# Kernel optimization log

Hardware: AMD Instinct MI355X
Metric: run time of the kernel (lower is better)

## Reference

```python
import jax, jax.numpy as jnp
import numpy as np

B, T, D = 2, 1024, 1024
H = 8            # num_heads
DK = 128         # head_k_dim
DV = 128         # head_v_dim
M = 128          # num_slots (== head_k_dim by default)
K = 32           # topk
EPS = 1e-5
SCALE = 1.0


def _rmsnorm(x, w, eps=EPS):
    return x * jax.lax.rsqrt(jnp.mean(x * x, axis=-1, keepdims=True) + eps) * w


def setup_inputs() -> dict:
    key = jax.random.key(0)
    ks = jax.random.split(key, 12)
    def lin(k, fan_in, fan_out):
        return jax.random.normal(k, (fan_in, fan_out), jnp.float32) / np.sqrt(fan_in).astype(np.float32)
    hidden_states = jax.random.normal(ks[0], (B, T, D), jnp.float32)
    Wq = lin(ks[1], D, H * DK)
    Wk = lin(ks[2], D, H * DK)
    Wv = lin(ks[3], D, H * DV)
    Wr = lin(ks[4], D, H * M)
    Wa = lin(ks[5], D, H)
    # Mamba2-style decay params
    A_log = jnp.log(jax.random.uniform(ks[6], (H,), jnp.float32, 1e-3, 16.0))
    dt = jnp.exp(jax.random.uniform(ks[7], (H,), jnp.float32) * (np.log(0.1) - np.log(0.001)) + np.log(0.001))
    dt = jnp.clip(dt, 1e-4, None)
    dt_bias = dt + jnp.log(-jnp.expm1(-dt))
    q_norm_w = jnp.ones((DK,), jnp.float32) + 0.01 * jax.random.normal(ks[8], (DK,), jnp.float32)
    k_norm_w = jnp.ones((DK,), jnp.float32) + 0.01 * jax.random.normal(ks[9], (DK,), jnp.float32)
    g_norm_w = jnp.ones((D,), jnp.float32) + 0.01 * jax.random.normal(ks[10], (D,), jnp.float32)
    Wo = lin(ks[11], H * DV, D)
    return dict(hidden_states=hidden_states, Wq=Wq, Wk=Wk, Wv=Wv, Wr=Wr, Wa=Wa,
                A_log=A_log, dt_bias=dt_bias, q_norm_w=q_norm_w, k_norm_w=k_norm_w,
                g_norm_w=g_norm_w, Wo=Wo)


def reference(hidden_states, Wq, Wk, Wv, Wr, Wa, A_log, dt_bias, q_norm_w, k_norm_w, g_norm_w, Wo):
    b, t, d = hidden_states.shape
    # projections
    q = (hidden_states @ Wq).reshape(b, t, H, DK)
    k = (hidden_states @ Wk).reshape(b, t, H, DK)
    v = jax.nn.silu((hidden_states @ Wv).reshape(b, t, H, DV))
    router = (hidden_states @ Wr).reshape(b, t, H, M)
    # Mamba2 decay (log-space, per head)
    f_head = -jnp.exp(A_log) * jax.nn.softplus(hidden_states @ Wa + dt_bias)  # [b,t,H]
    # swish feature map + per-head RMSNorm
    q = _rmsnorm(jax.nn.silu(q), q_norm_w)
    k = _rmsnorm(jax.nn.silu(k), k_norm_w)
    # sigmoid router scores, top-k slot routing (eval: no gumbel noise)
    scores = jax.nn.sigmoid(router)                    # [b,t,H,M]
    top_w, top_i = jax.lax.top_k(scores, K)            # [b,t,H,K]
    top_w = top_w / (jnp.sum(top_w, axis=-1, keepdims=True) + 1e-9)
    n = b * t * H
    rows = jnp.arange(n)[:, None]
    s_multihot = jnp.zeros((n, M), scores.dtype).at[rows, top_i.reshape(n, K)].set(
        top_w.reshape(n, K)).reshape(b, t, H, M)
    f = f_head[..., None] * s_multihot                 # [b,t,H,M], log decay per slot
    s = 1.0 - jnp.exp(f)                               # write gate per slot
    # decayed linear-attention recurrence over slots (M == DK):
    #   S_t[i,j] = exp(f_t[i]) * S_{t-1}[i,j] + s_t[i]*k_t[i]*v_t[j]
    #   o_t[j]   = scale * sum_i q_t[i] * S_t[i,j]
    def step(S, xs):
        q_t, k_t, v_t, f_t, s_t = xs                   # [b,H,*]
        S = jnp.exp(f_t)[..., None] * S + (s_t * k_t)[..., None] * v_t[..., None, :]
        o_t = jnp.einsum('bhk,bhkv->bhv', q_t, S) * SCALE
        return S, o_t
    xs = tuple(jnp.swapaxes(a, 0, 1) for a in (q, k, v, f, s))  # time-major
    S0 = jnp.zeros((b, H, DK, DV), q.dtype)
    _, o = jax.lax.scan(step, S0, xs)                  # o: [t,b,H,DV]
    o = jnp.swapaxes(o, 0, 1).reshape(b, t, H * DV)
    o = _rmsnorm(o, g_norm_w)                          # g_norm over hidden_size
    return o @ Wo
```

## Files before the change

kernel.cpp:

```cpp
#include <hip/hip_runtime.h>
#include <stdint.h>
#include <stddef.h>

#define H_ 8
#define T_ 1024

typedef __attribute__((ext_vector_type(8))) short s16x8;
typedef __attribute__((ext_vector_type(4))) float f32x4;
typedef __attribute__((ext_vector_type(16))) float f32x16;

static __device__ __forceinline__ unsigned short f2bf(float f){
  unsigned u = __float_as_uint(f);
  u += 0x7fffu + ((u >> 16) & 1u);
  return (unsigned short)(u >> 16);
}
static __device__ __forceinline__ float bf2f(unsigned short b){
  return __uint_as_float(((unsigned)b) << 16);
}
static __device__ __forceinline__ unsigned int pack_hl(float x){
  unsigned short h = f2bf(x);
  unsigned short l = f2bf(x - bf2f(h));
  return ((unsigned int)h << 16) | l;
}
static __device__ __forceinline__ void gl_lds16(const unsigned short* g, unsigned short* l){
  __builtin_amdgcn_global_load_lds((const __attribute__((address_space(1))) unsigned int*)g,
                                   (__attribute__((address_space(3))) unsigned int*)l,
                                   16, 0, 0);
}

__global__ void prep_k(const float* __restrict__ X, const float* __restrict__ Wa,
                       const float* __restrict__ A_log, const float* __restrict__ dtb,
                       unsigned short* __restrict__ hi, unsigned short* __restrict__ lo,
                       float* __restrict__ fh){
  __shared__ float xs[1024];
  int n = blockIdx.x, tid = threadIdx.x;
  size_t base = (size_t)n*1024 + tid*4;
  float4 x = *(const float4*)&X[base];
  *(float4*)&xs[tid*4] = x;
  float v[4] = {x.x,x.y,x.z,x.w};
  ushort4 h4, l4;
  unsigned short hh[4], ll[4];
#pragma unroll
  for(int j=0;j<4;j++){ hh[j]=f2bf(v[j]); ll[j]=f2bf(v[j]-bf2f(hh[j])); }
  h4.x=hh[0];h4.y=hh[1];h4.z=hh[2];h4.w=hh[3];
  l4.x=ll[0];l4.y=ll[1];l4.z=ll[2];l4.w=ll[3];
  *(ushort4*)&hi[base] = h4;
  *(ushort4*)&lo[base] = l4;
  __syncthreads();
  int h = tid>>5, l = tid&31;
  float s = 0.f;
  for(int k=l;k<1024;k+=32) s += xs[k]*Wa[(size_t)k*8 + h];
  s += __shfl_xor(s,1); s += __shfl_xor(s,2); s += __shfl_xor(s,4);
  s += __shfl_xor(s,8); s += __shfl_xor(s,16);
  if(l==0){
    float z = s + dtb[h];
    float sp = (z > 20.f) ? z : log1pf(expf(z));
    fh[(size_t)n*8 + h] = -expf(A_log[h]) * sp;
  }
}

__global__ void wtrans(const float* __restrict__ Wq, const float* __restrict__ Wk,
                       const float* __restrict__ Wv, const float* __restrict__ Wr,
                       const float* __restrict__ Wo,
                       unsigned short* __restrict__ WcatT3, unsigned short* __restrict__ WrThi,
                       unsigned short* __restrict__ WrTlo, unsigned short* __restrict__ WoT){
  __shared__ float tile[32][33];
  int z = blockIdx.z;
  const float* src = (z==0)?Wq:(z==1)?Wk:(z==2)?Wv:(z==3)?Wr:Wo;
  int c0 = blockIdx.x*32;
  int k0 = blockIdx.y*32;
  int tx = threadIdx.x, ty = threadIdx.y;
#pragma unroll
  for(int r=0;r<32;r+=8)
    tile[ty+r][tx] = src[(size_t)(k0+ty+r)*1024 + c0 + tx];
  __syncthreads();
#pragma unroll
  for(int r=0;r<32;r+=8){
    int c = c0 + ty + r;
    int k = k0 + tx;
    float v = tile[tx][ty+r];
    if(z < 3){
      WcatT3[((size_t)(z*1024 + c))*1024 + k] = f2bf(v);
    } else if(z == 3){
      unsigned short hv = f2bf(v);
      WrThi[(size_t)c*1024 + k] = hv;
      WrTlo[(size_t)c*1024 + k] = f2bf(v - bf2f(hv));
    } else {
      WoT[(size_t)c*1024 + k] = f2bf(v);
    }
  }
}

__launch_bounds__(256)
__global__ void gemm_fused(const unsigned short* __restrict__ Xhi, const unsigned short* __restrict__ Xlo,
                           const unsigned short* __restrict__ WcatT3, const unsigned short* __restrict__ WrThi,
                           const unsigned short* __restrict__ WrTlo,
                           float* __restrict__ C1, float* __restrict__ Rp){
  __shared__ unsigned short As[128*64];
  __shared__ unsigned short Bs[128*64];
  int bid = blockIdx.x;
  int blk = (bid&7)*96 + (bid>>3);
  const unsigned short *Ap, *Bp;
  float* Cout;
  int bx, by, N;
  if(blk < 384){
    bx = blk%24; by = blk/24; N = 3072;
    Ap = Xhi; Bp = WcatT3; Cout = C1;
  } else {
    int rb = blk-384;
    int seg = rb>>7, t2 = rb&127;
    bx = t2&7; by = t2>>3; N = 1024;
    Ap = (seg==2) ? Xlo : Xhi;
    Bp = (seg==1) ? WrTlo : WrThi;
    Cout = Rp + (size_t)seg*2048*1024;
  }
  int tid = threadIdx.x;
  int mBase = by*128, nBase = bx*128;
  int w = tid>>6, lane = tid&63, wr = w>>1, wc = w&1;
  int kg = lane>>4, l15 = lane&15;
  f32x4 acc[4][4];
#pragma unroll
  for(int i=0;i<4;i++)
#pragma unroll
    for(int j=0;j<4;j++) acc[i][j] = (f32x4){0.f,0.f,0.f,0.f};
  size_t aoff[4], boff[4];
#pragma unroll
  for(int p=0;p<4;p++){
    int c = p*256 + tid;
    int row = c>>3, sc = c&7, c8 = sc ^ (row&7);
    aoff[p] = (size_t)(mBase+row)*1024 + c8*8;
    boff[p] = (size_t)(nBase+row)*1024 + c8*8;
  }
  for(int kb=0; kb<1024; kb+=64){
#pragma unroll
    for(int p=0;p<4;p++){
      gl_lds16(Ap + aoff[p] + kb, &As[(p*256+tid)*8]);
      gl_lds16(Bp + boff[p] + kb, &Bs[(p*256+tid)*8]);
    }
    __syncthreads();
#pragma unroll
    for(int kk=0;kk<2;kk++){
      s16x8 afr[4], bfr[4];
#pragma unroll
      for(int f=0;f<4;f++){
        int rA = wr*64 + f*16 + l15;
        int rB = wc*64 + f*16 + l15;
        int cA = (kk*4 + kg) ^ (rA&7);
        int cB = (kk*4 + kg) ^ (rB&7);
        afr[f] = *(const s16x8*)&As[rA*64 + cA*8];
        bfr[f] = *(const s16x8*)&Bs[rB*64 + cB*8];
      }
#pragma unroll
      for(int fm=0;fm<4;fm++)
#pragma unroll
        for(int fn=0;fn<4;fn++)
          acc[fm][fn] = __builtin_amdgcn_mfma_f32_16x16x32_bf16(afr[fm], bfr[fn], acc[fm][fn], 0,0,0);
    }
    __syncthreads();
  }
#pragma unroll
  for(int fm=0;fm<4;fm++)
#pragma unroll
    for(int fn=0;fn<4;fn++){
      int col = nBase + wc*64 + fn*16 + l15;
      int row = mBase + wr*64 + fm*16 + kg*4;
#pragma unroll
      for(int r=0;r<4;r++) Cout[(size_t)(row+r)*N + col] = acc[fm][fn][r];
    }
}

__launch_bounds__(256)
__global__ void gemm_out(const unsigned short* __restrict__ A,
                         const unsigned short* __restrict__ BT,
                         float* __restrict__ C){
  __shared__ unsigned short As[128*64];
  __shared__ unsigned short Bs[64*64];
  const int K = 1024, N = 1024;
  int tid = threadIdx.x;
  int mBase = blockIdx.y*128, nBase = blockIdx.x*64;
  int w = tid>>6, lane = tid&63;
  int mh = w>>1, nh = w&1;
  int kg = lane>>4, l15 = lane&15;
  f32x4 acc[4][2];
#pragma unroll
  for(int i=0;i<4;i++)
#pragma unroll
    for(int j=0;j<2;j++) acc[i][j] = (f32x4){0.f,0.f,0.f,0.f};
  size_t aoff[4], boff[2];
#pragma unroll
  for(int p=0;p<4;p++){
    int c = p*256 + tid;
    int row = c>>3, sc = c&7, c8 = sc ^ (row&7);
    aoff[p] = (size_t)(mBase+row)*K + c8*8;
  }
#pragma unroll
  for(int p=0;p<2;p++){
    int c = p*256 + tid;
    int row = c>>3, sc = c&7, c8 = sc ^ (row&7);
    boff[p] = (size_t)(nBase+row)*K + c8*8;
  }
  for(int kb=0; kb<K; kb+=64){
#pragma unroll
    for(int p=0;p<4;p++) gl_lds16(A + aoff[p] + kb, &As[(p*256+tid)*8]);
#pragma unroll
    for(int p=0;p<2;p++) gl_lds16(BT + boff[p] + kb, &Bs[(p*256+tid)*8]);
    __syncthreads();
#pragma unroll
    for(int kk=0;kk<2;kk++){
      s16x8 afr[4], bfr[2];
#pragma unroll
      for(int f=0;f<4;f++){
        int r = mh*64 + f*16 + l15;
        afr[f] = *(const s16x8*)&As[r*64 + ((kk*4+kg) ^ (r&7))*8];
      }
#pragma unroll
      for(int f=0;f<2;f++){
        int r = nh*32 + f*16 + l15;
        bfr[f] = *(const s16x8*)&Bs[r*64 + ((kk*4+kg) ^ (r&7))*8];
      }
#pragma unroll
      for(int fm=0;fm<4;fm++)
#pragma unroll
        for(int fn=0;fn<2;fn++)
          acc[fm][fn] = __builtin_amdgcn_mfma_f32_16x16x32_bf16(afr[fm], bfr[fn], acc[fm][fn], 0,0,0);
    }
    __syncthreads();
  }
#pragma unroll
  for(int fm=0;fm<4;fm++)
#pragma unroll
    for(int fn=0;fn<2;fn++){
      int col = nBase + nh*32 + fn*16 + l15;
      int row = mBase + mh*64 + fm*16 + kg*4;
#pragma unroll
      for(int r=0;r<4;r++) C[(size_t)(row+r)*N + col] = acc[fm][fn][r];
    }
}

__launch_bounds__(256)
__global__ void postproc(const float* __restrict__ C1, const float* __restrict__ Rp,
                         const float* __restrict__ fh, const float* __restrict__ qw,
                         const float* __restrict__ kw,
                         float* __restrict__ Qd, float* __restrict__ Wt,
                         float* __restrict__ Fd, float* __restrict__ Vd){
  __shared__ unsigned long long keys[8][128];
  int n = blockIdx.x;
  int t = threadIdx.x;
  int b = n>>10, tt = n&1023;
  int h = t>>5;
  int i0 = (t&31)*4;
  size_t cb = (size_t)n*3072;
  size_t rbase = (size_t)n*1024 + h*128 + i0;
  float4 q4 = *(const float4*)&C1[cb + h*128 + i0];
  float4 k4 = *(const float4*)&C1[cb + 1024 + h*128 + i0];
  float4 v4 = *(const float4*)&C1[cb + 2048 + h*128 + i0];
  float4 r0 = *(const float4*)&Rp[rbase];
  float4 r1 = *(const float4*)&Rp[2048ull*1024 + rbase];
  float4 r2 = *(const float4*)&Rp[2ull*2048*1024 + rbase];
  float qv[4] = {q4.x,q4.y,q4.z,q4.w};
  float kv[4] = {k4.x,k4.y,k4.z,k4.w};
  float vv4[4] = {v4.x,v4.y,v4.z,v4.w};
  float rl[4] = {r0.x+r1.x+r2.x, r0.y+r1.y+r2.y, r0.z+r1.z+r2.z, r0.w+r1.w+r2.w};
  float qs[4], ks[4], vv[4], si[4];
  unsigned long long ki[4];
#pragma unroll
  for(int j=0;j<4;j++){
    qs[j] = qv[j]/(1.f+expf(-qv[j]));
    ks[j] = kv[j]/(1.f+expf(-kv[j]));
    vv[j] = vv4[j]/(1.f+expf(-vv4[j]));
    si[j] = 1.f/(1.f+expf(-rl[j]));
    ki[j] = (((unsigned long long)__float_as_uint(si[j])) << 7) | (unsigned)(127 - (i0+j));
    keys[h][i0+j] = ki[j];
  }
  __syncthreads();
  int cnt[4] = {0,0,0,0};
#pragma unroll 4
  for(int j=0;j<128;j+=2){
    ulonglong2 k2 = *(const ulonglong2*)&keys[h][j];
#pragma unroll
    for(int m=0;m<4;m++){
      cnt[m] += (k2.x > ki[m]);
      cnt[m] += (k2.y > ki[m]);
    }
  }
  bool sel[4];
#pragma unroll
  for(int m=0;m<4;m++) sel[m] = cnt[m] < 32;
  float x;
  x = qs[0]*qs[0]+qs[1]*qs[1]+qs[2]*qs[2]+qs[3]*qs[3];
  x+=__shfl_xor(x,1);x+=__shfl_xor(x,2);x+=__shfl_xor(x,4);x+=__shfl_xor(x,8);x+=__shfl_xor(x,16);
  float qrms = rsqrtf(x/128.f + 1e-5f);
  x = ks[0]*ks[0]+ks[1]*ks[1]+ks[2]*ks[2]+ks[3]*ks[3];
  x+=__shfl_xor(x,1);x+=__shfl_xor(x,2);x+=__shfl_xor(x,4);x+=__shfl_xor(x,8);x+=__shfl_xor(x,16);
  float krms = rsqrtf(x/128.f + 1e-5f);
  x = (sel[0]?si[0]:0.f)+(sel[1]?si[1]:0.f)+(sel[2]?si[2]:0.f)+(sel[3]?si[3]:0.f);
  x+=__shfl_xor(x,1);x+=__shfl_xor(x,2);x+=__shfl_xor(x,4);x+=__shfl_xor(x,8);x+=__shfl_xor(x,16);
  float winv = 1.f/(x + 1e-9f);
  float fhv = fh[(size_t)n*8 + h];
  size_t base = ((size_t)((b*H_ + h)*T_) + tt)*128 + i0;
  float4 qo, wo, fo, vo;
  float qd[4], wd[4], fd[4];
#pragma unroll
  for(int j=0;j<4;j++){
    float wgt = sel[j] ? si[j]*winv : 0.f;
    float f = fhv * wgt;
    qd[j] = qs[j]*qrms*qw[i0+j];
    wd[j] = (1.f - expf(f)) * (ks[j]*krms*kw[i0+j]);
    fd[j] = f;
  }
  qo.x=qd[0];qo.y=qd[1];qo.z=qd[2];qo.w=qd[3];
  wo.x=wd[0];wo.y=wd[1];wo.z=wd[2];wo.w=wd[3];
  fo.x=fd[0];fo.y=fd[1];fo.z=fd[2];fo.w=fd[3];
  vo.x=vv[0];vo.y=vv[1];vo.z=vv[2];vo.w=vv[3];
  *(float4*)&Qd[base] = qo;
  *(float4*)&Wt[base] = wo;
  *(float4*)&Fd[base] = fo;
  *(float4*)&Vd[base] = vo;
}

__launch_bounds__(256)
__global__ void chunk_sum(float* __restrict__ Fd, const float* __restrict__ Wt,
                          const float* __restrict__ Vd, float* __restrict__ dS,
                          float* __restrict__ E){
  __shared__ float Fc[32][132];
  __shared__ float Kh[32][132];
  int blk = blockIdx.x, bh = blk>>5, c = blk&31;
  int tid = threadIdx.x;
  int w = tid>>6, lane = tid&63;
  size_t fbase = ((size_t)bh*T_ + (size_t)c*32)*128;
#pragma unroll
  for(int v=0; v<4; v++){
    int e = v*1024 + tid*4;
    int t2 = e>>7, i0 = e&127;
    float4 f4 = *(const float4*)&Fd[fbase + e];
    *(float4*)&Fc[t2][i0] = f4;
  }
  __syncthreads();
  if(tid < 128){
    float a = 0.f;
    for(int t2=0;t2<32;t2++){ a += Fc[t2][tid]; Fc[t2][tid] = a; }
  }
  __syncthreads();
#pragma unroll
  for(int v=0; v<4; v++){
    int e = v*1024 + tid*4;
    int t2 = e>>7, i0 = e&127;
    float4 fc4 = *(const float4*)&Fc[t2][i0];
    *(float4*)&Fd[fbase + e] = fc4;
    float4 ft  = *(const float4*)&Fc[31][i0];
    float4 w4  = *(const float4*)&Wt[fbase + e];
    float4 kh;
    kh.x = w4.x * expf(ft.x - fc4.x);
    kh.y = w4.y * expf(ft.y - fc4.y);
    kh.z = w4.z * expf(ft.z - fc4.z);
    kh.w = w4.w * expf(ft.w - fc4.w);
    *(float4*)&Kh[t2][i0] = kh;
  }
  if(tid < 128) E[((size_t)bh*32 + c)*128 + tid] = expf(Fc[31][tid]);
  __syncthreads();
  int ig = lane>>3, jg = lane&7;
  const float* Vp = Vd + fbase;
  f32x4 acc[4][4];
#pragma unroll
  for(int a=0;a<4;a++)
#pragma unroll
    for(int q=0;q<4;q++) acc[a][q] = (f32x4){0.f,0.f,0.f,0.f};
#pragma unroll 4
  for(int t2=0;t2<32;t2++){
    float4 kq = *(const float4*)&Kh[t2][w*32 + ig*4];
    float4 v0 = *(const float4*)&Vp[t2*128 + jg*4];
    float4 v1 = *(const float4*)&Vp[t2*128 + jg*4 + 32];
    float4 v2 = *(const float4*)&Vp[t2*128 + jg*4 + 64];
    float4 v3 = *(const float4*)&Vp[t2*128 + jg*4 + 96];
    float kk[4] = {kq.x,kq.y,kq.z,kq.w};
#pragma unroll
    for(int a=0;a<4;a++){
      acc[a][0] += kk[a]*(f32x4){v0.x,v0.y,v0.z,v0.w};
      acc[a][1] += kk[a]*(f32x4){v1.x,v1.y,v1.z,v1.w};
      acc[a][2] += kk[a]*(f32x4){v2.x,v2.y,v2.z,v2.w};
      acc[a][3] += kk[a]*(f32x4){v3.x,v3.y,v3.z,v3.w};
    }
  }
  size_t dbase = (size_t)blk*16384;
#pragma unroll
  for(int q=0;q<4;q++)
#pragma unroll
    for(int jj=0;jj<4;jj++){
      float4 o4 = make_float4(acc[0][q][jj],acc[1][q][jj],acc[2][q][jj],acc[3][q][jj]);
      *(float4*)&dS[dbase + (size_t)(jg*4 + 32*q + jj)*128 + w*32 + ig*4] = o4;
    }
}

__global__ void scan_k(float* __restrict__ dS, const float* __restrict__ E){
  int g = blockIdx.x*256 + threadIdx.x;
  int bh = g>>12;
  int e4 = (g&4095)*4;
  int i0 = e4 & 127;
  float4 S = make_float4(0.f,0.f,0.f,0.f);
  for(int c=0;c<32;c++){
    size_t off = ((size_t)(bh*32 + c))*16384 + e4;
    float4 d   = *(const float4*)&dS[off];
    float4 Ec  = *(const float4*)&E[((size_t)(bh*32 + c))*128 + i0];
    *(float4*)&dS[off] = S;
    S.x = Ec.x*S.x + d.x;
    S.y = Ec.y*S.y + d.y;
    S.z = Ec.z*S.z + d.z;
    S.w = Ec.w*S.w + d.w;
  }
}

__launch_bounds__(256)
__global__ void chunk_out(const float* __restrict__ Qd, const float* __restrict__ Wt,
                          const float* __restrict__ Fd, const float* __restrict__ Vd,
                          const float* __restrict__ ST, float* __restrict__ O){
  __shared__ unsigned int qtP[32][132];
  __shared__ unsigned int ktP[32][132];
  __shared__ unsigned int Vt[128][36];
  __shared__ float Amat[32][40];
  int blk = blockIdx.x, bh = blk>>5, c = blk&31;
  int b = bh>>3, h = bh&7;
  int tid = threadIdx.x, w = tid>>6, lane = tid&63;
  int m = lane&31, hi = lane>>5;
  size_t fbase = ((size_t)bh*T_ + (size_t)c*32)*128;
#pragma unroll
  for(int p=0;p<4;p++){
    int e = p*1024 + tid*4;
    int t2 = e>>7, i0 = e&127;
    float4 f4 = *(const float4*)&Fd[fbase + e];
    float4 q4 = *(const float4*)&Qd[fbase + e];
    float4 w4 = *(const float4*)&Wt[fbase + e];
    float fv[4] = {f4.x,f4.y,f4.z,f4.w};
    float qv[4] = {q4.x,q4.y,q4.z,q4.w};
    float wv[4] = {w4.x,w4.y,w4.z,w4.w};
    uint4 qp, kp;
    unsigned int qa[4], ka[4];
#pragma unroll
    for(int j=0;j<4;j++){
      float ef = expf(fv[j]);
      qa[j] = pack_hl(qv[j]*ef);
      ka[j] = pack_hl(wv[j]/ef);
    }
    qp.x=qa[0]; qp.y=qa[1]; qp.z=qa[2]; qp.w=qa[3];
    kp.x=ka[0]; kp.y=ka[1]; kp.z=ka[2]; kp.w=ka[3];
    *(uint4*)&qtP[t2][i0] = qp;
    *(uint4*)&ktP[t2][i0] = kp;
  }
  {
    int n = tid&127, th = (tid>>7)*16;
    unsigned int vp[16];
#pragma unroll
    for(int j=0;j<16;j++) vp[j] = pack_hl(Vd[fbase + (size_t)(th+j)*128 + n]);
#pragma unroll
    for(int j=0;j<16;j+=4){
      uint4 v4; v4.x=vp[j]; v4.y=vp[j+1]; v4.z=vp[j+2]; v4.w=vp[j+3];
      *(uint4*)&Vt[n][th+j] = v4;
    }
  }
  __syncthreads();
  if(w == 0){
    f32x16 am;
#pragma unroll
    for(int r=0;r<16;r++) am[r] = 0.f;
#pragma unroll
    for(int s=0;s<8;s++){
      int ko = s*16 + hi*8;
      uint4 qa = *(const uint4*)&qtP[m][ko];
      uint4 qb = *(const uint4*)&qtP[m][ko+4];
      uint4 ka = *(const uint4*)&ktP[m][ko];
      uint4 kb = *(const uint4*)&ktP[m][ko+4];
      s16x8 qh, ql, kh, kl;
      unsigned int qw_[8] = {qa.x,qa.y,qa.z,qa.w,qb.x,qb.y,qb.z,qb.w};
      unsigned int kw_[8] = {ka.x,ka.y,ka.z,ka.w,kb.x,kb.y,kb.z,kb.w};
#pragma unroll
      for(int j=0;j<8;j++){
        qh[j]=(short)(qw_[j]>>16); ql[j]=(short)(qw_[j]&0xffff);
        kh[j]=(short)(kw_[j]>>16); kl[j]=(short)(kw_[j]&0xffff);
      }
      am = __builtin_amdgcn_mfma_f32_32x32x16_bf16(qh, kh, am, 0,0,0);
      am = __builtin_amdgcn_mfma_f32_32x32x16_bf16(qh, kl, am, 0,0,0);
      am = __builtin_amdgcn_mfma_f32_32x32x16_bf16(ql, kh, am, 0,0,0);
    }
#pragma unroll
    for(int r=0;r<16;r++){
      int rm = (r&3) + 8*(r>>2) + 4*hi;
      Amat[rm][m] = (m <= rm) ? am[r] : 0.f;
    }
  }
  f32x16 oacc;
#pragma unroll
  for(int r=0;r<16;r++) oacc[r] = 0.f;
  const float* Sp = ST + (size_t)blk*16384 + (size_t)(w*32 + m)*128;
#pragma unroll
  for(int s=0;s<8;s++){
    int ko = s*16 + hi*8;
    uint4 qa = *(const uint4*)&qtP[m][ko];
    uint4 qb = *(const uint4*)&qtP[m][ko+4];
    s16x8 qh, ql;
    unsigned int qw_[8] = {qa.x,qa.y,qa.z,qa.w,qb.x,qb.y,qb.z,qb.w};
#pragma unroll
    for(int j=0;j<8;j++){ qh[j]=(short)(qw_[j]>>16); ql[j]=(short)(qw_[j]&0xffff); }
    float4 s0 = *(const float4*)&Sp[ko];
    float4 s1 = *(const float4*)&Sp[ko+4];
    float sv[8] = {s0.x,s0.y,s0.z,s0.w,s1.x,s1.y,s1.z,s1.w};
    s16x8 sh, sl;
#pragma unroll
    for(int j=0;j<8;j++){
      unsigned short hh = f2bf(sv[j]);
      sh[j] = (short)hh; sl[j] = (short)f2bf(sv[j]-bf2f(hh));
    }
    oacc = __builtin_amdgcn_mfma_f32_32x32x16_bf16(qh, sh, oacc, 0,0,0);
    oacc = __builtin_amdgcn_mfma_f32_32x32x16_bf16(qh, sl, oacc, 0,0,0);
    oacc = __builtin_amdgcn_mfma_f32_32x32x16_bf16(ql, sh, oacc, 0,0,0);
  }
  __syncthreads();
#pragma unroll
  for(int s=0;s<2;s++){
    int uo = s*16 + hi*8;
    float4 a0 = *(const float4*)&Amat[m][uo];
    float4 a1 = *(const float4*)&Amat[m][uo+4];
    float av[8] = {a0.x,a0.y,a0.z,a0.w,a1.x,a1.y,a1.z,a1.w};
    s16x8 ah, al;
#pragma unroll
    for(int j=0;j<8;j++){
      unsigned short hh = f2bf(av[j]);
      ah[j] = (short)hh; al[j] = (short)f2bf(av[j]-bf2f(hh));
    }
    uint4 v0 = *(const uint4*)&Vt[w*32 + m][uo];
    uint4 v1 = *(const uint4*)&Vt[w*32 + m][uo+4];
    unsigned int vw[8] = {v0.x,v0.y,v0.z,v0.w,v1.x,v1.y,v1.z,v1.w};
    s16x8 vh, vl;
#pragma unroll
    for(int j=0;j<8;j++){ vh[j]=(short)(vw[j]>>16); vl[j]=(short)(vw[j]&0xffff); }
    oacc = __builtin_amdgcn_mfma_f32_32x32x16_bf16(ah, vh, oacc, 0,0,0);
    oacc = __builtin_amdgcn_mfma_f32_32x32x16_bf16(ah, vl, oacc, 0,0,0);
    oacc = __builtin_amdgcn_mfma_f32_32x32x16_bf16(al, vh, oacc, 0,0,0);
  }
#pragma unroll
  for(int r=0;r<16;r++){
    int tok = (r&3) + 8*(r>>2) + 4*hi;
    O[((size_t)(b*T_ + c*32 + tok))*1024 + h*128 + w*32 + m] = oacc[r];
  }
}

__global__ void gnorm_k(const float* __restrict__ Ob, const float* __restrict__ gw,
                        unsigned short* __restrict__ On){
  __shared__ float red[4];
  int n = blockIdx.x, tid = threadIdx.x;
  size_t base = (size_t)n*1024 + tid*4;
  float4 x = *(const float4*)&Ob[base];
  float ss = x.x*x.x + x.y*x.y + x.z*x.z + x.w*x.w;
  ss+=__shfl_xor(ss,1);ss+=__shfl_xor(ss,2);ss+=__shfl_xor(ss,4);
  ss+=__shfl_xor(ss,8);ss+=__shfl_xor(ss,16);ss+=__shfl_xor(ss,32);
  if((tid&63)==0) red[tid>>6]=ss;
  __syncthreads();
  float sc = rsqrtf((red[0]+red[1]+red[2]+red[3])/1024.f + 1e-5f);
  float4 g = *(const float4*)&gw[tid*4];
  ushort4 o4;
  o4.x=f2bf(x.x*sc*g.x); o4.y=f2bf(x.y*sc*g.y);
  o4.z=f2bf(x.z*sc*g.z); o4.w=f2bf(x.w*sc*g.w);
  *(ushort4*)&On[base]=o4;
}

extern "C" void kernel_launch(void* const* d_in, const int* in_sizes, int n_in,
                              void* d_out, int out_size, void* d_ws, size_t ws_size,
                              hipStream_t stream){
  const float* hs   = (const float*)d_in[0];
  const float* Wq   = (const float*)d_in[1];
  const float* Wk   = (const float*)d_in[2];
  const float* Wv   = (const float*)d_in[3];
  const float* Wr   = (const float*)d_in[4];
  const float* Wa   = (const float*)d_in[5];
  const float* A_log= (const float*)d_in[6];
  const float* dtb  = (const float*)d_in[7];
  const float* qw   = (const float*)d_in[8];
  const float* kw   = (const float*)d_in[9];
  const float* gw   = (const float*)d_in[10];
  const float* Wo   = (const float*)d_in[11];
  float* out = (float*)d_out;

  char* wsp = (char*)d_ws;
  size_t off = 0;
  auto alloc = [&](size_t bytes)->void*{ void* p = wsp + off; off += (bytes + 255) & ~(size_t)255; return p; };
  unsigned short* Xhi    = (unsigned short*)alloc(2048ull*1024*2);
  unsigned short* Xlo    = (unsigned short*)alloc(2048ull*1024*2);
  unsigned short* WcatT3 = (unsigned short*)alloc(3072ull*1024*2);
  unsigned short* WrThi  = (unsigned short*)alloc(1024ull*1024*2);
  unsigned short* WrTlo  = (unsigned short*)alloc(1024ull*1024*2);
  unsigned short* WoT    = (unsigned short*)alloc(1024ull*1024*2);
  float* C1 = (float*)alloc(2048ull*3072*4);
  float* fh = (float*)alloc(2048ull*8*4);
  float* Qd = (float*)alloc(16ull*1024*128*4);
  float* Wt = (float*)alloc(16ull*1024*128*4);
  float* Fd = (float*)alloc(16ull*1024*128*4);
  float* Vd = (float*)alloc(16ull*1024*128*4);
  float* E  = (float*)alloc(16ull*32*128*4);
  float* dS = (float*)alloc(16ull*32*16384*4);
  float* Ob = (float*)alloc(2048ull*1024*4);
  unsigned short* On = (unsigned short*)alloc(2048ull*1024*2);
  float* Rp = dS;
  (void)ws_size; (void)in_sizes; (void)n_in; (void)out_size;

  prep_k     <<<dim3(2048),        dim3(256),   0, stream>>>(hs, Wa, A_log, dtb, Xhi, Xlo, fh);
  wtrans     <<<dim3(32,32,5),     dim3(32,8),  0, stream>>>(Wq,Wk,Wv,Wr,Wo, WcatT3,WrThi,WrTlo,WoT);
  gemm_fused <<<dim3(768),         dim3(256),   0, stream>>>(Xhi, Xlo, WcatT3, WrThi, WrTlo, C1, Rp);
  postproc   <<<dim3(2048),        dim3(256),   0, stream>>>(C1, Rp, fh, qw, kw, Qd, Wt, Fd, Vd);
  chunk_sum  <<<dim3(512),         dim3(256),   0, stream>>>(Fd, Wt, Vd, dS, E);
  scan_k     <<<dim3(256),         dim3(256),   0, stream>>>(dS, E);
  chunk_out  <<<dim3(512),         dim3(256),   0, stream>>>(Qd, Wt, Fd, Vd, dS, Ob);
  gnorm_k    <<<dim3(2048),        dim3(256),   0, stream>>>(Ob, gw, On);
  gemm_out   <<<dim3(16,16),       dim3(256),   0, stream>>>(On, WoT, out);
}
```

Baseline: 254.0 us.

## Fuse postproc into chunk_sum and prefetch next chunk in scan

Merges the per-token postprocessing kernel (silu, RMSNorm, top-k routing, decay) into the chunk-sum kernel, so each block handles one (batch, head, chunk) and keeps F, gated K and V in shared memory. This avoids re-reading Fd, Wt and Vd from global memory and removes one launch. Rp gets its own buffer because it can no longer alias dS inside the same kernel. Top-k keys shrink to 32-bit by masking the low 7 mantissa bits, which could change tie-breaking among near-equal scores. The scan kernel also software-prefetches the next chunk's dS and E.

```diff
diff --git a/kernel.cpp b/kernel.cpp
--- a/kernel.cpp
+++ b/kernel.cpp
@@ -238,102 +238,100 @@
 }
 
 __launch_bounds__(256)
-__global__ void postproc(const float* __restrict__ C1, const float* __restrict__ Rp,
-                         const float* __restrict__ fh, const float* __restrict__ qw,
-                         const float* __restrict__ kw,
-                         float* __restrict__ Qd, float* __restrict__ Wt,
-                         float* __restrict__ Fd, float* __restrict__ Vd){
-  __shared__ unsigned long long keys[8][128];
-  int n = blockIdx.x;
-  int t = threadIdx.x;
-  int b = n>>10, tt = n&1023;
-  int h = t>>5;
-  int i0 = (t&31)*4;
-  size_t cb = (size_t)n*3072;
-  size_t rbase = (size_t)n*1024 + h*128 + i0;
-  float4 q4 = *(const float4*)&C1[cb + h*128 + i0];
-  float4 k4 = *(const float4*)&C1[cb + 1024 + h*128 + i0];
-  float4 v4 = *(const float4*)&C1[cb + 2048 + h*128 + i0];
-  float4 r0 = *(const float4*)&Rp[rbase];
-  float4 r1 = *(const float4*)&Rp[2048ull*1024 + rbase];
-  float4 r2 = *(const float4*)&Rp[2ull*2048*1024 + rbase];
-  float qv[4] = {q4.x,q4.y,q4.z,q4.w};
-  float kv[4] = {k4.x,k4.y,k4.z,k4.w};
-  float vv4[4] = {v4.x,v4.y,v4.z,v4.w};
-  float rl[4] = {r0.x+r1.x+r2.x, r0.y+r1.y+r2.y, r0.z+r1.z+r2.z, r0.w+r1.w+r2.w};
-  float qs[4], ks[4], vv[4], si[4];
-  unsigned long long ki[4];
-#pragma unroll
-  for(int j=0;j<4;j++){
-    qs[j] = qv[j]/(1.f+expf(-qv[j]));
-    ks[j] = kv[j]/(1.f+expf(-kv[j]));
-    vv[j] = vv4[j]/(1.f+expf(-vv4[j]));
-    si[j] = 1.f/(1.f+expf(-rl[j]));
-    ki[j] = (((unsigned long long)__float_as_uint(si[j])) << 7) | (unsigned)(127 - (i0+j));
-    keys[h][i0+j] = ki[j];
-  }
-  __syncthreads();
-  int cnt[4] = {0,0,0,0};
-#pragma unroll 4
-  for(int j=0;j<128;j+=2){
-    ulonglong2 k2 = *(const ulonglong2*)&keys[h][j];
-#pragma unroll
-    for(int m=0;m<4;m++){
-      cnt[m] += (k2.x > ki[m]);
-      cnt[m] += (k2.y > ki[m]);
-    }
-  }
-  bool sel[4];
-#pragma unroll
-  for(int m=0;m<4;m++) sel[m] = cnt[m] < 32;
-  float x;
-  x = qs[0]*qs[0]+qs[1]*qs[1]+qs[2]*qs[2]+qs[3]*qs[3];
-  x+=__shfl_xor(x,1);x+=__shfl_xor(x,2);x+=__shfl_xor(x,4);x+=__shfl_xor(x,8);x+=__shfl_xor(x,16);
-  float qrms = rsqrtf(x/128.f + 1e-5f);
-  x = ks[0]*ks[0]+ks[1]*ks[1]+ks[2]*ks[2]+ks[3]*ks[3];
-  x+=__shfl_xor(x,1);x+=__shfl_xor(x,2);x+=__shfl_xor(x,4);x+=__shfl_xor(x,8);x+=__shfl_xor(x,16);
-  float krms = rsqrtf(x/128.f + 1e-5f);
-  x = (sel[0]?si[0]:0.f)+(sel[1]?si[1]:0.f)+(sel[2]?si[2]:0.f)+(sel[3]?si[3]:0.f);
-  x+=__shfl_xor(x,1);x+=__shfl_xor(x,2);x+=__shfl_xor(x,4);x+=__shfl_xor(x,8);x+=__shfl_xor(x,16);
-  float winv = 1.f/(x + 1e-9f);
-  float fhv = fh[(size_t)n*8 + h];
-  size_t base = ((size_t)((b*H_ + h)*T_) + tt)*128 + i0;
-  float4 qo, wo, fo, vo;
-  float qd[4], wd[4], fd[4];
-#pragma unroll
-  for(int j=0;j<4;j++){
-    float wgt = sel[j] ? si[j]*winv : 0.f;
-    float f = fhv * wgt;
-    qd[j] = qs[j]*qrms*qw[i0+j];
-    wd[j] = (1.f - expf(f)) * (ks[j]*krms*kw[i0+j]);
-    fd[j] = f;
-  }
-  qo.x=qd[0];qo.y=qd[1];qo.z=qd[2];qo.w=qd[3];
-  wo.x=wd[0];wo.y=wd[1];wo.z=wd[2];wo.w=wd[3];
-  fo.x=fd[0];fo.y=fd[1];fo.z=fd[2];fo.w=fd[3];
-  vo.x=vv[0];vo.y=vv[1];vo.z=vv[2];vo.w=vv[3];
-  *(float4*)&Qd[base] = qo;
-  *(float4*)&Wt[base] = wo;
-  *(float4*)&Fd[base] = fo;
-  *(float4*)&Vd[base] = vo;
-}
-
-__launch_bounds__(256)
-__global__ void chunk_sum(float* __restrict__ Fd, const float* __restrict__ Wt,
-                          const float* __restrict__ Vd, float* __restrict__ dS,
-                          float* __restrict__ E){
+__global__ void pp_sum(const float* __restrict__ C1, const float* __restrict__ Rp,
+                       const float* __restrict__ fh, const float* __restrict__ qw,
+                       const float* __restrict__ kw,
+                       float* __restrict__ Qd, float* __restrict__ Wt,
+                       float* __restrict__ Fd, float* __restrict__ Vd,
+                       float* __restrict__ dS, float* __restrict__ E){
+  __shared__ unsigned scU[32][128];
   __shared__ float Fc[32][132];
   __shared__ float Kh[32][132];
+  __shared__ float Vs[32][132];
   int blk = blockIdx.x, bh = blk>>5, c = blk&31;
+  int b = bh>>3, h = bh&7;
   int tid = threadIdx.x;
-  int w = tid>>6, lane = tid&63;
+  int g = tid>>5, i0 = (tid&31)*4;
+  int n0 = b*1024 + c*32;
   size_t fbase = ((size_t)bh*T_ + (size_t)c*32)*128;
+  float si_r[4][4];
+  unsigned ki_r[4][4];
 #pragma unroll
   for(int v=0; v<4; v++){
-    int e = v*1024 + tid*4;
-    int t2 = e>>7, i0 = e&127;
-    float4 f4 = *(const float4*)&Fd[fbase + e];
-    *(float4*)&Fc[t2][i0] = f4;
+    int t2 = v*8 + g;
+    size_t rb = (size_t)(n0 + t2)*1024 + h*128 + i0;
+    float4 r0 = *(const float4*)&Rp[rb];
+    float4 r1 = *(const float4*)&Rp[2048ull*1024 + rb];
+    float4 r2 = *(const float4*)&Rp[2ull*2048*1024 + rb];
+    float rl[4] = {r0.x+r1.x+r2.x, r0.y+r1.y+r2.y, r0.z+r1.z+r2.z, r0.w+r1.w+r2.w};
+#pragma unroll
+    for(int j=0;j<4;j++){
+      float si = 1.f/(1.f+expf(-rl[j]));
+      si_r[v][j] = si;
+      ki_r[v][j] = (__float_as_uint(si) & ~127u) | (unsigned)(127 - (i0+j));
+      scU[t2][i0+j] = ki_r[v][j];
+    }
+  }
+  __syncthreads();
+#pragma unroll
+  for(int v=0; v<4; v++){
+    int t2 = v*8 + g;
+    int n = n0 + t2;
+    size_t cb = (size_t)n*3072 + h*128 + i0;
+    float4 q4 = *(const float4*)&C1[cb];
+    float4 k4 = *(const float4*)&C1[cb + 1024];
+    float4 v4 = *(const float4*)&C1[cb + 2048];
+    float qv[4]={q4.x,q4.y,q4.z,q4.w}, kv[4]={k4.x,k4.y,k4.z,k4.w}, vraw[4]={v4.x,v4.y,v4.z,v4.w};
+    float qs[4], ks[4], vv[4];
+#pragma unroll
+    for(int j=0;j<4;j++){
+      qs[j] = qv[j]/(1.f+expf(-qv[j]));
+      ks[j] = kv[j]/(1.f+expf(-kv[j]));
+      vv[j] = vraw[j]/(1.f+expf(-vraw[j]));
+    }
+    int cnt[4]={0,0,0,0};
+#pragma unroll 4
+    for(int j=0;j<128;j+=4){
+      uint4 kk4 = *(const uint4*)&scU[t2][j];
+      unsigned kk[4]={kk4.x,kk4.y,kk4.z,kk4.w};
+#pragma unroll
+      for(int m=0;m<4;m++)
+        cnt[m] += (int)(kk[0]>ki_r[v][m]) + (int)(kk[1]>ki_r[v][m])
+                + (int)(kk[2]>ki_r[v][m]) + (int)(kk[3]>ki_r[v][m]);
+    }
+    bool sel[4];
+#pragma unroll
+    for(int m=0;m<4;m++) sel[m] = cnt[m] < 32;
+    float x;
+    x = qs[0]*qs[0]+qs[1]*qs[1]+qs[2]*qs[2]+qs[3]*qs[3];
+    x+=__shfl_xor(x,1);x+=__shfl_xor(x,2);x+=__shfl_xor(x,4);x+=__shfl_xor(x,8);x+=__shfl_xor(x,16);
+    float qrms = rsqrtf(x/128.f + 1e-5f);
+    x = ks[0]*ks[0]+ks[1]*ks[1]+ks[2]*ks[2]+ks[3]*ks[3];
+    x+=__shfl_xor(x,1);x+=__shfl_xor(x,2);x+=__shfl_xor(x,4);x+=__shfl_xor(x,8);x+=__shfl_xor(x,16);
+    float krms = rsqrtf(x/128.f + 1e-5f);
+    x = (sel[0]?si_r[v][0]:0.f)+(sel[1]?si_r[v][1]:0.f)+(sel[2]?si_r[v][2]:0.f)+(sel[3]?si_r[v][3]:0.f);
+    x+=__shfl_xor(x,1);x+=__shfl_xor(x,2);x+=__shfl_xor(x,4);x+=__shfl_xor(x,8);x+=__shfl_xor(x,16);
+    float winv = 1.f/(x + 1e-9f);
+    float fhv = fh[(size_t)n*8 + h];
+    float qd[4], wd[4], fd[4];
+#pragma unroll
+    for(int j=0;j<4;j++){
+      float wgt = sel[j] ? si_r[v][j]*winv : 0.f;
+      float f = fhv * wgt;
+      qd[j] = qs[j]*qrms*qw[i0+j];
+      wd[j] = (1.f - expf(f)) * (ks[j]*krms*kw[i0+j]);
+      fd[j] = f;
+    }
+    size_t basev = fbase + (size_t)t2*128 + i0;
+    float4 qo; qo.x=qd[0];qo.y=qd[1];qo.z=qd[2];qo.w=qd[3];
+    float4 wo; wo.x=wd[0];wo.y=wd[1];wo.z=wd[2];wo.w=wd[3];
+    float4 vo; vo.x=vv[0];vo.y=vv[1];vo.z=vv[2];vo.w=vv[3];
+    *(float4*)&Qd[basev] = qo;
+    *(float4*)&Wt[basev] = wo;
+    *(float4*)&Vd[basev] = vo;
+    *(float4*)&Fc[t2][i0] = make_float4(fd[0],fd[1],fd[2],fd[3]);
+    *(float4*)&Kh[t2][i0] = wo;
+    *(float4*)&Vs[t2][i0] = vo;
   }
   __syncthreads();
   if(tid < 128){
@@ -344,22 +342,21 @@
 #pragma unroll
   for(int v=0; v<4; v++){
     int e = v*1024 + tid*4;
-    int t2 = e>>7, i0 = e&127;
-    float4 fc4 = *(const float4*)&Fc[t2][i0];
+    int t2 = e>>7, i2 = e&127;
+    float4 fc4 = *(const float4*)&Fc[t2][i2];
     *(float4*)&Fd[fbase + e] = fc4;
-    float4 ft  = *(const float4*)&Fc[31][i0];
-    float4 w4  = *(const float4*)&Wt[fbase + e];
-    float4 kh;
-    kh.x = w4.x * expf(ft.x - fc4.x);
-    kh.y = w4.y * expf(ft.y - fc4.y);
-    kh.z = w4.z * expf(ft.z - fc4.z);
-    kh.w = w4.w * expf(ft.w - fc4.w);
-    *(float4*)&Kh[t2][i0] = kh;
+    float4 ft  = *(const float4*)&Fc[31][i2];
+    float4 kh  = *(const float4*)&Kh[t2][i2];
+    kh.x *= expf(ft.x - fc4.x);
+    kh.y *= expf(ft.y - fc4.y);
+    kh.z *= expf(ft.z - fc4.z);
+    kh.w *= expf(ft.w - fc4.w);
+    *(float4*)&Kh[t2][i2] = kh;
   }
   if(tid < 128) E[((size_t)bh*32 + c)*128 + tid] = expf(Fc[31][tid]);
   __syncthreads();
+  int w = tid>>6, lane = tid&63;
   int ig = lane>>3, jg = lane&7;
-  const float* Vp = Vd + fbase;
   f32x4 acc[4][4];
 #pragma unroll
   for(int a=0;a<4;a++)
@@ -368,10 +365,10 @@
 #pragma unroll 4
   for(int t2=0;t2<32;t2++){
     float4 kq = *(const float4*)&Kh[t2][w*32 + ig*4];
-    float4 v0 = *(const float4*)&Vp[t2*128 + jg*4];
-    float4 v1 = *(const float4*)&Vp[t2*128 + jg*4 + 32];
-    float4 v2 = *(const float4*)&Vp[t2*128 + jg*4 + 64];
-    float4 v3 = *(const float4*)&Vp[t2*128 + jg*4 + 96];
+    float4 v0 = *(const float4*)&Vs[t2][jg*4];
+    float4 v1 = *(const float4*)&Vs[t2][jg*4 + 32];
+    float4 v2 = *(const float4*)&Vs[t2][jg*4 + 64];
+    float4 v3 = *(const float4*)&Vs[t2][jg*4 + 96];
     float kk[4] = {kq.x,kq.y,kq.z,kq.w};
 #pragma unroll
     for(int a=0;a<4;a++){
@@ -396,16 +393,23 @@
   int bh = g>>12;
   int e4 = (g&4095)*4;
   int i0 = e4 & 127;
+  size_t base  = (size_t)bh*32*16384 + e4;
+  size_t ebase = (size_t)bh*32*128 + i0;
   float4 S = make_float4(0.f,0.f,0.f,0.f);
+  float4 d  = *(const float4*)&dS[base];
+  float4 Ec = *(const float4*)&E[ebase];
   for(int c=0;c<32;c++){
-    size_t off = ((size_t)(bh*32 + c))*16384 + e4;
-    float4 d   = *(const float4*)&dS[off];
-    float4 Ec  = *(const float4*)&E[((size_t)(bh*32 + c))*128 + i0];
-    *(float4*)&dS[off] = S;
+    float4 dn = make_float4(0,0,0,0), En = make_float4(0,0,0,0);
+    if(c < 31){
+      dn = *(const float4*)&dS[base + (size_t)(c+1)*16384];
+      En = *(const float4*)&E[ebase + (size_t)(c+1)*128];
+    }
+    *(float4*)&dS[base + (size_t)c*16384] = S;
     S.x = Ec.x*S.x + d.x;
     S.y = Ec.y*S.y + d.y;
     S.z = Ec.z*S.z + d.z;
     S.w = Ec.w*S.w + d.w;
+    d = dn; Ec = En;
   }
 }
 
@@ -588,6 +592,7 @@
   unsigned short* WrTlo  = (unsigned short*)alloc(1024ull*1024*2);
   unsigned short* WoT    = (unsigned short*)alloc(1024ull*1024*2);
   float* C1 = (float*)alloc(2048ull*3072*4);
+  float* Rp = (float*)alloc(3ull*2048*1024*4);
   float* fh = (float*)alloc(2048ull*8*4);
   float* Qd = (float*)alloc(16ull*1024*128*4);
   float* Wt = (float*)alloc(16ull*1024*128*4);
@@ -597,14 +602,12 @@
   float* dS = (float*)alloc(16ull*32*16384*4);
   float* Ob = (float*)alloc(2048ull*1024*4);
   unsigned short* On = (unsigned short*)alloc(2048ull*1024*2);
-  float* Rp = dS;
   (void)ws_size; (void)in_sizes; (void)n_in; (void)out_size;
 
   prep_k     <<<dim3(2048),        dim3(256),   0, stream>>>(hs, Wa, A_log, dtb, Xhi, Xlo, fh);
   wtrans     <<<dim3(32,32,5),     dim3(32,8),  0, stream>>>(Wq,Wk,Wv,Wr,Wo, WcatT3,WrThi,WrTlo,WoT);
   gemm_fused <<<dim3(768),         dim3(256),   0, stream>>>(Xhi, Xlo, WcatT3, WrThi, WrTlo, C1, Rp);
-  postproc   <<<dim3(2048),        dim3(256),   0, stream>>>(C1, Rp, fh, qw, kw, Qd, Wt, Fd, Vd);
-  chunk_sum  <<<dim3(512),         dim3(256),   0, stream>>>(Fd, Wt, Vd, dS, E);
+  pp_sum     <<<dim3(512),         dim3(256),   0, stream>>>(C1, Rp, fh, qw, kw, Qd, Wt, Fd, Vd, dS, E);
   scan_k     <<<dim3(256),         dim3(256),   0, stream>>>(dS, E);
   chunk_out  <<<dim3(512),         dim3(256),   0, stream>>>(Qd, Wt, Fd, Vd, dS, Ob);
   gnorm_k    <<<dim3(2048),        dim3(256),   0, stream>>>(Ob, gw, On);
```

Result: no change. 251.1 us (-1.1%).
